# Kernel tuning notes

Hardware: AMD Instinct MI355X
Metric: run time of the kernel (lower is better)

## Reference

```python
import jax, jax.numpy as jnp
import numpy as np

B, SS, T, D, H = 512, 4, 64, 300, 256  # batch, sentences/sample, words/sentence, wordvec, hidden


def setup_inputs() -> dict:
    key = jax.random.key(0)
    ks = jax.random.split(key, 17)
    s = 0.05
    rn = lambda k, shape: (jax.random.normal(k, shape, jnp.float32) * s)
    return dict(
        x=jax.random.normal(ks[0], (B, SS, T, D), jnp.float32),
        # gru1: GRU(300 -> 256), PyTorch gate order (r, z, n)
        w_ih1=rn(ks[1], (3 * H, D)), w_hh1=rn(ks[2], (3 * H, H)),
        b_ih1=rn(ks[3], (3 * H,)), b_hh1=rn(ks[4], (3 * H,)),
        # gru2: bidirectional GRU(256 -> 256), forward + backward directions
        w_ih2f=rn(ks[5], (3 * H, H)), w_hh2f=rn(ks[6], (3 * H, H)),
        b_ih2f=rn(ks[7], (3 * H,)), b_hh2f=rn(ks[8], (3 * H,)),
        w_ih2b=rn(ks[9], (3 * H, H)), w_hh2b=rn(ks[10], (3 * H, H)),
        b_ih2b=rn(ks[11], (3 * H,)), b_hh2b=rn(ks[12], (3 * H,)),
        # classifier: Linear(512,256) -> LeakyReLU(0.1) -> Linear(256,2)
        wc1=rn(ks[13], (H, 2 * H)), bc1=rn(ks[14], (H,)),
        wc2=rn(ks[15], (2, H)), bc2=rn(ks[16], (2,)),
    )


def _gru_final_hidden(x, w_ih, w_hh, b_ih, b_hh):
    # x: [N, T, D] -> final hidden state [N, H]; PyTorch GRU math, gate order r,z,n
    xg = jnp.einsum('ntd,gd->tng', x, w_ih) + b_ih  # [T, N, 3H], input gates precomputed
    h0 = jnp.zeros((x.shape[0], w_hh.shape[1]), x.dtype)

    def step(h, xg_t):
        hg = h @ w_hh.T + b_hh
        xr, xz, xn = jnp.split(xg_t, 3, axis=-1)
        hr, hz, hn = jnp.split(hg, 3, axis=-1)
        r = jax.nn.sigmoid(xr + hr)
        z = jax.nn.sigmoid(xz + hz)
        n = jnp.tanh(xn + r * hn)
        return (1.0 - z) * n + z * h, None

    hT, _ = jax.lax.scan(step, h0, xg)
    return hT


def _gru_cell_zero_h(x, w_ih, b_ih, b_hh):
    # gru2 is called with seq_len=1 and h0=0, so each direction is one cell step
    # (W_hh @ 0 == 0, only the hidden biases survive)
    xg = x @ w_ih.T + b_ih
    xr, xz, xn = jnp.split(xg, 3, axis=-1)
    br, bz, bn = jnp.split(b_hh, 3)
    r = jax.nn.sigmoid(xr + br)
    z = jax.nn.sigmoid(xz + bz)
    n = jnp.tanh(xn + r * bn)
    return (1.0 - z) * n


def reference(x, w_ih1, w_hh1, b_ih1, b_hh1,
              w_ih2f, w_hh2f, b_ih2f, b_hh2f,
              w_ih2b, w_hh2b, b_ih2b, b_hh2b,
              wc1, bc1, wc2, bc2):
    Bn, S, Tn, Dn = x.shape
    # integrate_words: gru1 over each sentence's words, keep final hidden
    h1 = _gru_final_hidden(x.reshape(Bn * S, Tn, Dn), w_ih1, w_hh1, b_ih1, b_hh1)
    h1 = h1.reshape(Bn, S, -1)  # [B, SS, H]
    # integrate_sentences: bidir gru2 with batch=SS, seq_len=1; out[SS//2] is kept,
    # and with seq_len=1 that output depends only on the middle sentence's embedding
    mid = h1[:, S // 2, :]  # [B, H]
    hf = _gru_cell_zero_h(mid, w_ih2f, b_ih2f, b_hh2f)
    hb = _gru_cell_zero_h(mid, w_ih2b, b_ih2b, b_hh2b)
    emb = jnp.concatenate([hf, hb], axis=-1)  # [B, 2H]
    pre = emb @ wc1.T + bc1
    hidden = jnp.where(pre >= 0, pre, 0.1 * pre)  # LeakyReLU(0.1)
    logits = hidden @ wc2.T + bc2  # [B, 2]
    return logits
```

## Files before the change

### kernel.cpp

```cpp
#include <hip/hip_runtime.h>
#include <hip/hip_bf16.h>

typedef unsigned short u16;
typedef unsigned int u32;
using short8 = __attribute__((ext_vector_type(8))) short;
using f32x4  = __attribute__((ext_vector_type(4))) float;

#define T_   64
#define D_   300
#define H_   256
#define G_   768
#define NROW 512
#define M_   (NROW * T_)
#define KP_  320

__device__ __forceinline__ float bf2f(u16 v) {
    union { u32 u; float f; } x; x.u = ((u32)v) << 16; return x.f;
}
__device__ __forceinline__ u16 f2bf(float f) {
    union { u32 u; float f; } x; x.f = f;
    u32 u = x.u;
    u32 r = (u + 0x7FFFu + ((u >> 16) & 1u)) >> 16;
    return (u16)r;
}
__device__ __forceinline__ float frcp(float x) {
    float r; asm("v_rcp_f32 %0, %1" : "=v"(r) : "v"(x)); return r;
}
__device__ __forceinline__ float fsigm(float x) { return frcp(1.f + __expf(-x)); }
__device__ __forceinline__ float ftanh(float x) {
    return 1.f - 2.f * frcp(1.f + __expf(2.f * x));
}
__device__ __forceinline__ float sigm(float x) { return 1.f / (1.f + expf(-x)); }

__global__ __launch_bounds__(256) void kx_cast(
    const float* __restrict__ x, u16* __restrict__ xb)
{
    const int gid = blockIdx.x * 256 + threadIdx.x;
    const int row = gid / 40, seg = gid - row * 40;
    const int k0 = seg * 8;
    const int n = row >> 6, t = row & 63;
    const float* src = x + (size_t)(n * 256 + 128 + t) * D_;
    union { u16 h[8]; uint4 q; } u;
    if (k0 + 8 <= D_) {
        const float4 a = *reinterpret_cast<const float4*>(src + k0);
        const float4 b = *reinterpret_cast<const float4*>(src + k0 + 4);
        u.h[0] = f2bf(a.x); u.h[1] = f2bf(a.y); u.h[2] = f2bf(a.z); u.h[3] = f2bf(a.w);
        u.h[4] = f2bf(b.x); u.h[5] = f2bf(b.y); u.h[6] = f2bf(b.z); u.h[7] = f2bf(b.w);
    } else {
#pragma unroll
        for (int e = 0; e < 8; ++e)
            u.h[e] = (k0 + e < D_) ? f2bf(src[k0 + e]) : (u16)0;
    }
    *reinterpret_cast<uint4*>(&xb[(size_t)row * KP_ + k0]) = u.q;
}

__global__ __launch_bounds__(256) void k0_prep(
    const float* __restrict__ w_ih1, const float* __restrict__ w_hh1,
    const float* __restrict__ b_ih1, const float* __restrict__ b_hh1,
    const float* __restrict__ w2f, const float* __restrict__ w2b,
    const float* __restrict__ wc1,
    u16* __restrict__ wihb, u16* __restrict__ whpk,
    u16* __restrict__ w2ft, u16* __restrict__ w2bt, u16* __restrict__ wc1t,
    float* __restrict__ biasc)
{
    int y = blockIdx.y;
    int tid = blockIdx.x * 256 + threadIdx.x;
    if (y == 0) {
        if (tid < G_ * KP_) {
            int g = tid / KP_, k = tid % KP_;
            wihb[tid] = (k < D_) ? f2bf(w_ih1[g * D_ + k]) : (u16)0;
        }
    } else if (y == 1) {
        if (tid < 48 * 8 * 64) {
            int lane = tid & 63;
            int ks = (tid >> 6) & 7;
            int nt = tid >> 9;
            int g  = nt * 16 + (lane & 15);
            int kb = ks * 32 + ((lane >> 4) << 3);
            union { u16 h[8]; uint4 q; } u;
#pragma unroll
            for (int e = 0; e < 8; ++e) u.h[e] = f2bf(w_hh1[g * H_ + kb + e]);
            *reinterpret_cast<uint4*>(&whpk[(size_t)tid * 8]) = u.q;
        }
    } else if (y == 2 || y == 3) {
        if (tid < G_ * H_) {
            int k = tid / G_, g = tid % G_;
            const float* src = (y == 2) ? w2f : w2b;
            u16* dst = (y == 2) ? w2ft : w2bt;
            dst[tid] = f2bf(src[g * H_ + k]);
        }
    } else {
        if (tid < 512 * 256) {
            int k = tid / 256, o = tid % 256;
            wc1t[tid] = f2bf(wc1[o * 512 + k]);
        }
        if (tid < G_)
            biasc[tid] = b_ih1[tid] + (tid < 2 * H_ ? b_hh1[tid] : 0.f);
    }
}

__global__ __launch_bounds__(256) void k1_xgemm(
    const u16* __restrict__ xb, const u16* __restrict__ wihb,
    const float* __restrict__ biasc, u16* __restrict__ xg)
{
    __shared__ alignas(16) u16 As[128 * 40];
    __shared__ alignas(16) u16 Bs[128 * 40];
    const int tid = threadIdx.x;
    const int l = tid & 63, wv = tid >> 6;
    const int wrow = wv >> 1, wcol = wv & 1;
    const int row0 = blockIdx.x * 128, col0 = blockIdx.y * 128;

    f32x4 acc[4][4];
#pragma unroll
    for (int i = 0; i < 4; ++i)
#pragma unroll
        for (int j = 0; j < 4; ++j) acc[i][j] = (f32x4){0.f, 0.f, 0.f, 0.f};

    const int ar = tid >> 1, ah = tid & 1;
    const u16* xrow  = xb + (size_t)(row0 + ar) * KP_;
    const u16* wrowp = wihb + (size_t)(col0 + ar) * KP_;

    for (int k0 = 0; k0 < KP_; k0 += 32) {
        *reinterpret_cast<uint4*>(&As[ar * 40 + ah * 16]) =
            *reinterpret_cast<const uint4*>(xrow + k0 + ah * 16);
        *reinterpret_cast<uint4*>(&As[ar * 40 + ah * 16 + 8]) =
            *reinterpret_cast<const uint4*>(xrow + k0 + ah * 16 + 8);
        *reinterpret_cast<uint4*>(&Bs[ar * 40 + ah * 16]) =
            *reinterpret_cast<const uint4*>(wrowp + k0 + ah * 16);
        *reinterpret_cast<uint4*>(&Bs[ar * 40 + ah * 16 + 8]) =
            *reinterpret_cast<const uint4*>(wrowp + k0 + ah * 16 + 8);
        __syncthreads();

        short8 af[4], bf[4];
#pragma unroll
        for (int fi = 0; fi < 4; ++fi)
            af[fi] = *reinterpret_cast<const short8*>(
                &As[(wrow * 64 + fi * 16 + (l & 15)) * 40 + ((l >> 4) << 3)]);
#pragma unroll
        for (int fj = 0; fj < 4; ++fj)
            bf[fj] = *reinterpret_cast<const short8*>(
                &Bs[(wcol * 64 + fj * 16 + (l & 15)) * 40 + ((l >> 4) << 3)]);
#pragma unroll
        for (int fi = 0; fi < 4; ++fi)
#pragma unroll
            for (int fj = 0; fj < 4; ++fj)
                acc[fi][fj] = __builtin_amdgcn_mfma_f32_16x16x32_bf16(
                    af[fi], bf[fj], acc[fi][fj], 0, 0, 0);
        __syncthreads();
    }

    float bias[4];
#pragma unroll
    for (int fj = 0; fj < 4; ++fj)
        bias[fj] = biasc[col0 + wcol * 64 + fj * 16 + (l & 15)];
#pragma unroll
    for (int fi = 0; fi < 4; ++fi)
#pragma unroll
        for (int fj = 0; fj < 4; ++fj)
#pragma unroll
            for (int q = 0; q < 4; ++q) {
                int row = row0 + wrow * 64 + fi * 16 + ((l >> 4) << 2) + q;
                int col = col0 + wcol * 64 + fj * 16 + (l & 15);
                xg[((size_t)(row & 63) * NROW + (row >> 6)) * G_ + col] =
                    f2bf(acc[fi][fj][q] + bias[fj]);
            }
}

#define PIN_W asm volatile("" : \
    "+v"(wr[0][0]),"+v"(wr[0][1]),"+v"(wr[0][2]),"+v"(wr[0][3]),"+v"(wr[0][4]),"+v"(wr[0][5]), \
    "+v"(wr[1][0]),"+v"(wr[1][1]),"+v"(wr[1][2]),"+v"(wr[1][3]),"+v"(wr[1][4]),"+v"(wr[1][5]), \
    "+v"(wr[2][0]),"+v"(wr[2][1]),"+v"(wr[2][2]),"+v"(wr[2][3]),"+v"(wr[2][4]),"+v"(wr[2][5]), \
    "+v"(wr[3][0]),"+v"(wr[3][1]),"+v"(wr[3][2]),"+v"(wr[3][3]),"+v"(wr[3][4]),"+v"(wr[3][5]), \
    "+v"(wr[4][0]),"+v"(wr[4][1]),"+v"(wr[4][2]),"+v"(wr[4][3]),"+v"(wr[4][4]),"+v"(wr[4][5]), \
    "+v"(wr[5][0]),"+v"(wr[5][1]),"+v"(wr[5][2]),"+v"(wr[5][3]),"+v"(wr[5][4]),"+v"(wr[5][5]))

__global__ __launch_bounds__(512)
__attribute__((amdgpu_waves_per_eu(2, 2)))
void k2_gru(const u16* __restrict__ xg, const u16* __restrict__ whpk,
            const float* __restrict__ b_hh, float* __restrict__ mid)
{
    extern __shared__ u16 smem[];
    u16* wl = smem;
    u16* hb = smem + 48 * 2 * 64 * 8;
    const int tid = threadIdx.x;
    const int l = tid & 63, wv = tid >> 6;
    const int n0 = blockIdx.x * 16;
    const int col = l & 15, rgrp = l >> 4;
    const int arow = col, klo = rgrp << 3;

    short8 wr[6][6];
#pragma unroll
    for (int gt = 0; gt < 3; ++gt)
#pragma unroll
        for (int a = 0; a < 2; ++a) {
            const int nt = gt * 16 + wv * 2 + a;
#pragma unroll
            for (int ks = 0; ks < 6; ++ks)
                wr[gt * 2 + a][ks] = *reinterpret_cast<const short8*>(
                    &whpk[(size_t)((nt * 8 + ks) * 64 + l) * 8]);
        }
    for (int c = tid; c < 48 * 2 * 64; c += 512) {
        const int nt = c >> 7, j = (c >> 6) & 1, ll = c & 63;
        *reinterpret_cast<uint4*>(&wl[(size_t)c * 8]) =
            *reinterpret_cast<const uint4*>(
                &whpk[(size_t)((nt * 8 + 6 + j) * 64 + ll) * 8]);
    }
    for (int i = tid; i < 16 * 264 / 2; i += 512) ((u32*)hb)[i] = 0;

    float bhn[2];
    u32 xo[2][4];
#pragma unroll
    for (int a = 0; a < 2; ++a) {
        const int ju = wv * 32 + a * 16 + col;
        bhn[a] = b_hh[512 + ju];
#pragma unroll
        for (int q = 0; q < 4; ++q)
            xo[a][q] = (u32)(rgrp * 4 + q) * G_ + ju;
    }
    float h[2][4] = {};
    const u16* xgn = xg + (size_t)n0 * G_;

    __syncthreads();

    for (int t = 0; t < T_; ++t) {
        PIN_W;

        u32 xv[3][2][4];
        const u16* xt = xgn + (size_t)t * ((size_t)NROW * G_);
#pragma unroll
        for (int a = 0; a < 2; ++a)
#pragma unroll
            for (int q = 0; q < 4; ++q) {
                xv[0][a][q] = xt[xo[a][q]];
                xv[1][a][q] = xt[xo[a][q] + 256];
                xv[2][a][q] = xt[xo[a][q] + 512];
            }

        f32x4 acc[6];
#pragma unroll
        for (int m = 0; m < 6; ++m) acc[m] = (f32x4){0.f, 0.f, 0.f, 0.f};
        __builtin_amdgcn_s_setprio(1);
#pragma unroll
        for (int ks = 0; ks < 6; ++ks) {
            const short8 afr = *reinterpret_cast<const short8*>(
                &hb[arow * 264 + ks * 32 + klo]);
#pragma unroll
            for (int m = 0; m < 6; ++m)
                acc[m] = __builtin_amdgcn_mfma_f32_16x16x32_bf16(
                    afr, wr[m][ks], acc[m], 0, 0, 0);
        }
#pragma unroll
        for (int ks = 6; ks < 8; ++ks) {
            const short8 afr = *reinterpret_cast<const short8*>(
                &hb[arow * 264 + ks * 32 + klo]);
#pragma unroll
            for (int gt = 0; gt < 3; ++gt)
#pragma unroll
                for (int a = 0; a < 2; ++a) {
                    const int nt2 = (gt * 16 + wv * 2 + a) * 2 + (ks - 6);
                    const short8 bfr = *reinterpret_cast<const short8*>(
                        &wl[(size_t)(nt2 * 64 + l) * 8]);
                    acc[gt * 2 + a] = __builtin_amdgcn_mfma_f32_16x16x32_bf16(
                        afr, bfr, acc[gt * 2 + a], 0, 0, 0);
                }
        }
        __builtin_amdgcn_s_setprio(0);

        asm volatile("s_waitcnt lgkmcnt(0)" ::: "memory");
        __builtin_amdgcn_sched_barrier(0);
        __builtin_amdgcn_s_barrier();
        __builtin_amdgcn_sched_barrier(0);

#pragma unroll
        for (int a = 0; a < 2; ++a)
#pragma unroll
            for (int q = 0; q < 4; ++q) {
                const float xr = bf2f((u16)xv[0][a][q]);
                const float xz = bf2f((u16)xv[1][a][q]);
                const float xn = bf2f((u16)xv[2][a][q]);
                const float rg = fsigm(xr + acc[0 + a][q]);
                const float zg = fsigm(xz + acc[2 + a][q]);
                const float ng = ftanh(xn + rg * (acc[4 + a][q] + bhn[a]));
                h[a][q] = zg * (h[a][q] - ng) + ng;
                hb[(rgrp * 4 + q) * 264 + wv * 32 + a * 16 + col] = f2bf(h[a][q]);
            }

        asm volatile("s_waitcnt lgkmcnt(0)" ::: "memory");
        __builtin_amdgcn_sched_barrier(0);
        __builtin_amdgcn_s_barrier();
        __builtin_amdgcn_sched_barrier(0);
    }

#pragma unroll
    for (int a = 0; a < 2; ++a)
#pragma unroll
        for (int q = 0; q < 4; ++q)
            mid[(size_t)(n0 + rgrp * 4 + q) * H_ + wv * 32 + a * 16 + col] = h[a][q];
}

__global__ __launch_bounds__(256) void k3_head(
    const float* __restrict__ mid,
    const u16* __restrict__ w2ft, const u16* __restrict__ w2bt,
    const float* __restrict__ b_ih2f, const float* __restrict__ b_hh2f,
    const float* __restrict__ b_ih2b, const float* __restrict__ b_hh2b,
    const u16* __restrict__ wc1t, const float* __restrict__ bc1,
    const float* __restrict__ wc2, const float* __restrict__ bc2,
    float* __restrict__ out)
{
    __shared__ float m[4][H_];
    __shared__ float xg2[2][4][G_];
    __shared__ float emb[4][512];
    __shared__ float hid[4][H_];
    int tid = threadIdx.x;
    int r0 = blockIdx.x * 4;

    for (int i = tid; i < 4 * H_; i += 256) {
        int r = i >> 8, k = i & 255;
        m[r][k] = mid[(size_t)(r0 + r) * H_ + k];
    }
    __syncthreads();

    const int g0 = tid, g1 = tid + 256, g2 = tid + 512;
    float bf0 = b_ih2f[g0] + b_hh2f[g0];
    float bf1 = b_ih2f[g1] + b_hh2f[g1];
    float bf2v = b_ih2f[g2];
    float bb0 = b_ih2b[g0] + b_hh2b[g0];
    float bb1 = b_ih2b[g1] + b_hh2b[g1];
    float bb2v = b_ih2b[g2];
    float af[4][3], ab[4][3];
#pragma unroll
    for (int r = 0; r < 4; ++r) {
        af[r][0] = bf0; af[r][1] = bf1; af[r][2] = bf2v;
        ab[r][0] = bb0; ab[r][1] = bb1; ab[r][2] = bb2v;
    }
#pragma unroll 4
    for (int k = 0; k < H_; ++k) {
        float wf0 = bf2f(w2ft[k * G_ + g0]);
        float wf1 = bf2f(w2ft[k * G_ + g1]);
        float wf2 = bf2f(w2ft[k * G_ + g2]);
        float wb0 = bf2f(w2bt[k * G_ + g0]);
        float wb1 = bf2f(w2bt[k * G_ + g1]);
        float wb2 = bf2f(w2bt[k * G_ + g2]);
#pragma unroll
        for (int r = 0; r < 4; ++r) {
            float mm = m[r][k];
            af[r][0] += mm * wf0; af[r][1] += mm * wf1; af[r][2] += mm * wf2;
            ab[r][0] += mm * wb0; ab[r][1] += mm * wb1; ab[r][2] += mm * wb2;
        }
    }
#pragma unroll
    for (int r = 0; r < 4; ++r) {
        xg2[0][r][g0] = af[r][0]; xg2[0][r][g1] = af[r][1]; xg2[0][r][g2] = af[r][2];
        xg2[1][r][g0] = ab[r][0]; xg2[1][r][g1] = ab[r][1]; xg2[1][r][g2] = ab[r][2];
    }
    __syncthreads();

    {
        const int j = tid;
        float bnf = b_hh2f[512 + j], bnb = b_hh2b[512 + j];
#pragma unroll
        for (int r = 0; r < 4; ++r) {
            float rg = sigm(xg2[0][r][j]);
            float zg = sigm(xg2[0][r][256 + j]);
            float ng = tanhf(xg2[0][r][512 + j] + rg * bnf);
            emb[r][j] = (1.f - zg) * ng;
            rg = sigm(xg2[1][r][j]);
            zg = sigm(xg2[1][r][256 + j]);
            ng = tanhf(xg2[1][r][512 + j] + rg * bnb);
            emb[r][256 + j] = (1.f - zg) * ng;
        }
    }
    __syncthreads();

    {
        const int o = tid;
        float acc[4];
        float b = bc1[o];
#pragma unroll
        for (int r = 0; r < 4; ++r) acc[r] = b;
#pragma unroll 4
        for (int k = 0; k < 512; ++k) {
            float w = bf2f(wc1t[k * H_ + o]);
#pragma unroll
            for (int r = 0; r < 4; ++r) acc[r] += emb[r][k] * w;
        }
#pragma unroll
        for (int r = 0; r < 4; ++r) {
            float pre = acc[r];
            hid[r][o] = pre >= 0.f ? pre : 0.1f * pre;
        }
    }
    __syncthreads();

    {
        int grp = tid >> 5, lane = tid & 31;
        int r = grp >> 1, cc = grp & 1;
        float s = 0.f;
        for (int k = lane; k < H_; k += 32) s += hid[r][k] * wc2[cc * H_ + k];
#pragma unroll
        for (int msk = 16; msk >= 1; msk >>= 1) s += __shfl_xor(s, msk, 32);
        if (lane == 0) out[(size_t)(r0 + r) * 2 + cc] = s + bc2[cc];
    }
}

extern "C" void kernel_launch(void* const* d_in, const int* in_sizes, int n_in,
                              void* d_out, int out_size, void* d_ws, size_t ws_size,
                              hipStream_t stream)
{
    const float* x      = (const float*)d_in[0];
    const float* w_ih1  = (const float*)d_in[1];
    const float* w_hh1  = (const float*)d_in[2];
    const float* b_ih1  = (const float*)d_in[3];
    const float* b_hh1  = (const float*)d_in[4];
    const float* w_ih2f = (const float*)d_in[5];
    const float* b_ih2f = (const float*)d_in[7];
    const float* b_hh2f = (const float*)d_in[8];
    const float* w_ih2b = (const float*)d_in[9];
    const float* b_ih2b = (const float*)d_in[11];
    const float* b_hh2b = (const float*)d_in[12];
    const float* wc1    = (const float*)d_in[13];
    const float* bc1    = (const float*)d_in[14];
    const float* wc2    = (const float*)d_in[15];
    const float* bc2    = (const float*)d_in[16];
    float* out = (float*)d_out;

    char* p = (char*)d_ws;
    u16* xg   = (u16*)p;  p += (size_t)M_ * G_ * 2;
    u16* xb   = (u16*)p;  p += (size_t)M_ * KP_ * 2;
    u16* wihb = (u16*)p;  p += (size_t)G_ * KP_ * 2;
    u16* whpk = (u16*)p;  p += (size_t)48 * 8 * 64 * 8 * 2;
    u16* w2ft = (u16*)p;  p += (size_t)G_ * H_ * 2;
    u16* w2bt = (u16*)p;  p += (size_t)G_ * H_ * 2;
    u16* wc1t = (u16*)p;  p += (size_t)512 * 256 * 2;
    float* mid = (float*)p; p += (size_t)NROW * H_ * 4;
    float* biasc = (float*)p; p += (size_t)G_ * 4;

    kx_cast<<<M_ * 40 / 256, 256, 0, stream>>>(x, xb);
    k0_prep<<<dim3(960, 5), 256, 0, stream>>>(w_ih1, w_hh1, b_ih1, b_hh1,
                                              w_ih2f, w_ih2b, wc1,
                                              wihb, whpk, w2ft, w2bt, wc1t, biasc);
    k1_xgemm<<<dim3(M_ / 128, G_ / 128), 256, 0, stream>>>(xb, wihb, biasc, xg);
    const int k2_lds = (48 * 2 * 64 * 8 + 16 * 264) * 2;
    k2_gru<<<32, 512, k2_lds, stream>>>(xg, whpk, b_hh1, mid);
    k3_head<<<128, 256, 0, stream>>>(mid, w2ft, w2bt, b_ih2f, b_hh2f,
                                     b_ih2b, b_hh2b, wc1t, bc1, wc2, bc2, out);
}
```

Before: 269.8 us.

## Double-buffer GRU hidden state, pack gate inputs per lane, pin weights in AGPRs

The input-gate projection output is re-laid out so that each GRU lane's six r/z/n values for its two units sit contiguously, which lets them load as three 32-bit words instead of twelve scattered 16-bit loads. The hidden-state LDS buffer is double-buffered, removing one of the two barriers per timestep. The recurrent weight fragments are pinned in AGPRs once before the loop, replacing the per-step VGPR pin. The costs are a scattered store pattern in the GEMM epilogue and more LDS use.

```diff
diff --git a/kernel.cpp b/kernel.cpp
--- a/kernel.cpp
+++ b/kernel.cpp
@@ -16,6 +16,12 @@
 
 __device__ __forceinline__ float bf2f(u16 v) {
     union { u32 u; float f; } x; x.u = ((u32)v) << 16; return x.f;
+}
+__device__ __forceinline__ float bf2f_lo(u32 w) {
+    union { u32 u; float f; } x; x.u = w << 16; return x.f;
+}
+__device__ __forceinline__ float bf2f_hi(u32 w) {
+    union { u32 u; float f; } x; x.u = w & 0xFFFF0000u; return x.f;
 }
 __device__ __forceinline__ u16 f2bf(float f) {
     union { u32 u; float f; } x; x.f = f;
@@ -101,7 +107,7 @@
 
 __global__ __launch_bounds__(256) void k1_xgemm(
     const u16* __restrict__ xb, const u16* __restrict__ wihb,
-    const float* __restrict__ biasc, u16* __restrict__ xg)
+    const float* __restrict__ biasc, u16* __restrict__ xgp)
 {
     __shared__ alignas(16) u16 As[128 * 40];
     __shared__ alignas(16) u16 Bs[128 * 40];
@@ -156,27 +162,24 @@
 #pragma unroll
     for (int fi = 0; fi < 4; ++fi)
 #pragma unroll
-        for (int fj = 0; fj < 4; ++fj)
+        for (int fj = 0; fj < 4; ++fj) {
+            const int cg = col0 + wcol * 64 + fj * 16 + (l & 15);
+            const int gate = cg >> 8, unit = cg & 255;
+            const int wv8 = unit >> 5, a = (unit >> 4) & 1, c = unit & 15;
 #pragma unroll
             for (int q = 0; q < 4; ++q) {
-                int row = row0 + wrow * 64 + fi * 16 + ((l >> 4) << 2) + q;
-                int col = col0 + wcol * 64 + fj * 16 + (l & 15);
-                xg[((size_t)(row & 63) * NROW + (row >> 6)) * G_ + col] =
-                    f2bf(acc[fi][fj][q] + bias[fj]);
+                const int row = row0 + wrow * 64 + fi * 16 + ((l >> 4) << 2) + q;
+                const int t = row & 63, n = row >> 6;
+                const size_t idx =
+                    (((size_t)t * NROW + n) * 128 + wv8 * 16 + c) * 6 + a * 3 + gate;
+                xgp[idx] = f2bf(acc[fi][fj][q] + bias[fj]);
             }
-}
-
-#define PIN_W asm volatile("" : \
-    "+v"(wr[0][0]),"+v"(wr[0][1]),"+v"(wr[0][2]),"+v"(wr[0][3]),"+v"(wr[0][4]),"+v"(wr[0][5]), \
-    "+v"(wr[1][0]),"+v"(wr[1][1]),"+v"(wr[1][2]),"+v"(wr[1][3]),"+v"(wr[1][4]),"+v"(wr[1][5]), \
-    "+v"(wr[2][0]),"+v"(wr[2][1]),"+v"(wr[2][2]),"+v"(wr[2][3]),"+v"(wr[2][4]),"+v"(wr[2][5]), \
-    "+v"(wr[3][0]),"+v"(wr[3][1]),"+v"(wr[3][2]),"+v"(wr[3][3]),"+v"(wr[3][4]),"+v"(wr[3][5]), \
-    "+v"(wr[4][0]),"+v"(wr[4][1]),"+v"(wr[4][2]),"+v"(wr[4][3]),"+v"(wr[4][4]),"+v"(wr[4][5]), \
-    "+v"(wr[5][0]),"+v"(wr[5][1]),"+v"(wr[5][2]),"+v"(wr[5][3]),"+v"(wr[5][4]),"+v"(wr[5][5]))
+        }
+}
 
 __global__ __launch_bounds__(512)
 __attribute__((amdgpu_waves_per_eu(2, 2)))
-void k2_gru(const u16* __restrict__ xg, const u16* __restrict__ whpk,
+void k2_gru(const u16* __restrict__ xgp, const u16* __restrict__ whpk,
             const float* __restrict__ b_hh, float* __restrict__ mid)
 {
     extern __shared__ u16 smem[];
@@ -199,43 +202,46 @@
                 wr[gt * 2 + a][ks] = *reinterpret_cast<const short8*>(
                     &whpk[(size_t)((nt * 8 + ks) * 64 + l) * 8]);
         }
+    asm volatile("" :
+        "+a"(wr[0][0]),"+a"(wr[0][1]),"+a"(wr[0][2]),"+a"(wr[0][3]),"+a"(wr[0][4]),"+a"(wr[0][5]),
+        "+a"(wr[1][0]),"+a"(wr[1][1]),"+a"(wr[1][2]),"+a"(wr[1][3]),"+a"(wr[1][4]),"+a"(wr[1][5]),
+        "+a"(wr[2][0]),"+a"(wr[2][1]),"+a"(wr[2][2]),"+a"(wr[2][3]),"+a"(wr[2][4]),"+a"(wr[2][5]));
+    asm volatile("" :
+        "+a"(wr[3][0]),"+a"(wr[3][1]),"+a"(wr[3][2]),"+a"(wr[3][3]),"+a"(wr[3][4]),"+a"(wr[3][5]),
+        "+a"(wr[4][0]),"+a"(wr[4][1]),"+a"(wr[4][2]),"+a"(wr[4][3]),"+a"(wr[4][4]),"+a"(wr[4][5]),
+        "+a"(wr[5][0]),"+a"(wr[5][1]),"+a"(wr[5][2]),"+a"(wr[5][3]),"+a"(wr[5][4]),"+a"(wr[5][5]));
+
     for (int c = tid; c < 48 * 2 * 64; c += 512) {
         const int nt = c >> 7, j = (c >> 6) & 1, ll = c & 63;
         *reinterpret_cast<uint4*>(&wl[(size_t)c * 8]) =
             *reinterpret_cast<const uint4*>(
                 &whpk[(size_t)((nt * 8 + 6 + j) * 64 + ll) * 8]);
     }
-    for (int i = tid; i < 16 * 264 / 2; i += 512) ((u32*)hb)[i] = 0;
+    for (int i = tid; i < 2 * 16 * 264 / 2; i += 512) ((u32*)hb)[i] = 0;
 
     float bhn[2];
-    u32 xo[2][4];
-#pragma unroll
-    for (int a = 0; a < 2; ++a) {
-        const int ju = wv * 32 + a * 16 + col;
-        bhn[a] = b_hh[512 + ju];
-#pragma unroll
-        for (int q = 0; q < 4; ++q)
-            xo[a][q] = (u32)(rgrp * 4 + q) * G_ + ju;
-    }
+    u32 xo[4];
+#pragma unroll
+    for (int a = 0; a < 2; ++a)
+        bhn[a] = b_hh[512 + wv * 32 + a * 16 + col];
+#pragma unroll
+    for (int q = 0; q < 4; ++q)
+        xo[q] = ((u32)(n0 + rgrp * 4 + q) * 128 + wv * 16 + col) * 6;
     float h[2][4] = {};
-    const u16* xgn = xg + (size_t)n0 * G_;
 
     __syncthreads();
 
+    int p = 0;
     for (int t = 0; t < T_; ++t) {
-        PIN_W;
-
-        u32 xv[3][2][4];
-        const u16* xt = xgn + (size_t)t * ((size_t)NROW * G_);
-#pragma unroll
-        for (int a = 0; a < 2; ++a)
-#pragma unroll
-            for (int q = 0; q < 4; ++q) {
-                xv[0][a][q] = xt[xo[a][q]];
-                xv[1][a][q] = xt[xo[a][q] + 256];
-                xv[2][a][q] = xt[xo[a][q] + 512];
-            }
-
+        u32 pw0[4], pw1[4], pw2[4];
+        const u16* xt = xgp + (size_t)t * ((size_t)NROW * 128 * 6);
+#pragma unroll
+        for (int q = 0; q < 4; ++q) {
+            const u32* pp = reinterpret_cast<const u32*>(xt + xo[q]);
+            pw0[q] = pp[0]; pw1[q] = pp[1]; pw2[q] = pp[2];
+        }
+
+        const u16* hbr = hb + p * (16 * 264);
         f32x4 acc[6];
 #pragma unroll
         for (int m = 0; m < 6; ++m) acc[m] = (f32x4){0.f, 0.f, 0.f, 0.f};
@@ -243,7 +249,7 @@
 #pragma unroll
         for (int ks = 0; ks < 6; ++ks) {
             const short8 afr = *reinterpret_cast<const short8*>(
-                &hb[arow * 264 + ks * 32 + klo]);
+                &hbr[arow * 264 + ks * 32 + klo]);
 #pragma unroll
             for (int m = 0; m < 6; ++m)
                 acc[m] = __builtin_amdgcn_mfma_f32_16x16x32_bf16(
@@ -252,7 +258,7 @@
 #pragma unroll
         for (int ks = 6; ks < 8; ++ks) {
             const short8 afr = *reinterpret_cast<const short8*>(
-                &hb[arow * 264 + ks * 32 + klo]);
+                &hbr[arow * 264 + ks * 32 + klo]);
 #pragma unroll
             for (int gt = 0; gt < 3; ++gt)
 #pragma unroll
@@ -266,29 +272,30 @@
         }
         __builtin_amdgcn_s_setprio(0);
 
+        u16* hbw = hb + (p ^ 1) * (16 * 264);
+#pragma unroll
+        for (int q = 0; q < 4; ++q) {
+            {
+                const float rg = fsigm(bf2f_lo(pw0[q]) + acc[0][q]);
+                const float zg = fsigm(bf2f_hi(pw0[q]) + acc[2][q]);
+                const float ng = ftanh(bf2f_lo(pw1[q]) + rg * (acc[4][q] + bhn[0]));
+                h[0][q] = zg * (h[0][q] - ng) + ng;
+                hbw[(rgrp * 4 + q) * 264 + wv * 32 + col] = f2bf(h[0][q]);
+            }
+            {
+                const float rg = fsigm(bf2f_hi(pw1[q]) + acc[1][q]);
+                const float zg = fsigm(bf2f_lo(pw2[q]) + acc[3][q]);
+                const float ng = ftanh(bf2f_hi(pw2[q]) + rg * (acc[5][q] + bhn[1]));
+                h[1][q] = zg * (h[1][q] - ng) + ng;
+                hbw[(rgrp * 4 + q) * 264 + wv * 32 + 16 + col] = f2bf(h[1][q]);
+            }
+        }
+
         asm volatile("s_waitcnt lgkmcnt(0)" ::: "memory");
         __builtin_amdgcn_sched_barrier(0);
         __builtin_amdgcn_s_barrier();
         __builtin_amdgcn_sched_barrier(0);
-
-#pragma unroll
-        for (int a = 0; a < 2; ++a)
-#pragma unroll
-            for (int q = 0; q < 4; ++q) {
-                const float xr = bf2f((u16)xv[0][a][q]);
-                const float xz = bf2f((u16)xv[1][a][q]);
-                const float xn = bf2f((u16)xv[2][a][q]);
-                const float rg = fsigm(xr + acc[0 + a][q]);
-                const float zg = fsigm(xz + acc[2 + a][q]);
-                const float ng = ftanh(xn + rg * (acc[4 + a][q] + bhn[a]));
-                h[a][q] = zg * (h[a][q] - ng) + ng;
-                hb[(rgrp * 4 + q) * 264 + wv * 32 + a * 16 + col] = f2bf(h[a][q]);
-            }
-
-        asm volatile("s_waitcnt lgkmcnt(0)" ::: "memory");
-        __builtin_amdgcn_sched_barrier(0);
-        __builtin_amdgcn_s_barrier();
-        __builtin_amdgcn_sched_barrier(0);
+        p ^= 1;
     }
 
 #pragma unroll
@@ -425,7 +432,7 @@
     float* out = (float*)d_out;
 
     char* p = (char*)d_ws;
-    u16* xg   = (u16*)p;  p += (size_t)M_ * G_ * 2;
+    u16* xgp  = (u16*)p;  p += (size_t)M_ * 768 * 2;
     u16* xb   = (u16*)p;  p += (size_t)M_ * KP_ * 2;
     u16* wihb = (u16*)p;  p += (size_t)G_ * KP_ * 2;
     u16* whpk = (u16*)p;  p += (size_t)48 * 8 * 64 * 8 * 2;
@@ -439,9 +446,9 @@
     k0_prep<<<dim3(960, 5), 256, 0, stream>>>(w_ih1, w_hh1, b_ih1, b_hh1,
                                               w_ih2f, w_ih2b, wc1,
                                               wihb, whpk, w2ft, w2bt, wc1t, biasc);
-    k1_xgemm<<<dim3(M_ / 128, G_ / 128), 256, 0, stream>>>(xb, wihb, biasc, xg);
-    const int k2_lds = (48 * 2 * 64 * 8 + 16 * 264) * 2;
-    k2_gru<<<32, 512, k2_lds, stream>>>(xg, whpk, b_hh1, mid);
+    k1_xgemm<<<dim3(M_ / 128, G_ / 128), 256, 0, stream>>>(xb, wihb, biasc, xgp);
+    const int k2_lds = (48 * 2 * 64 * 8 + 2 * 16 * 264) * 2;
+    k2_gru<<<32, 512, k2_lds, stream>>>(xgp, whpk, b_hh1, mid);
     k3_head<<<128, 256, 0, stream>>>(mid, w2ft, w2bt, b_ih2f, b_hh2f,
                                      b_ih2b, b_hh2b, wc1t, bc1, wc2, bc2, out);
 }
```

New measurement: 255.0 us. -5.5%, faster.
